# Kernel optimization log

Hardware: AMD Instinct MI355X
Metric: run time of the kernel (lower is better)

The kernel has to match this reference:

```python
import jax, jax.numpy as jnp
import numpy as np

H = 4096          # hidden_size
I = 11008         # intermediate_size
B, S = 4, 2048    # batch, seq_len


def _dequant(wq, scale):
    # per-output-channel symmetric int8 dequant: [out,in] int * [out] scale
    return wq.astype(jnp.float32) * scale[:, None]


def setup_inputs() -> dict:
    key = jax.random.key(0)
    ks = jax.random.split(key, 7)
    x = jax.random.normal(ks[0], (B, S, H), dtype=jnp.float32)
    gate_wq = jax.random.randint(ks[1], (I, H), -127, 128, dtype=jnp.int32)
    up_wq = jax.random.randint(ks[2], (I, H), -127, 128, dtype=jnp.int32)
    down_wq = jax.random.randint(ks[3], (H, I), -127, 128, dtype=jnp.int32)
    # realistic small per-channel scales (~1/127 of a unit-ish weight range)
    gate_scale = jax.random.uniform(ks[4], (I,), dtype=jnp.float32) * 0.01 + 1e-4
    up_scale = jax.random.uniform(ks[5], (I,), dtype=jnp.float32) * 0.01 + 1e-4
    down_scale = jax.random.uniform(ks[6], (H,), dtype=jnp.float32) * 0.01 + 1e-4
    return {
        "x": x,
        "gate_wq": gate_wq, "gate_scale": gate_scale,
        "up_wq": up_wq, "up_scale": up_scale,
        "down_wq": down_wq, "down_scale": down_scale,
    }


def reference(x, gate_wq, gate_scale, up_wq, up_scale, down_wq, down_scale):
    # y = down( gate(x) * up(x) )  -- NOTE: source forward has no activation fn
    gate_w = _dequant(gate_wq, gate_scale)   # [I, H]
    up_w = _dequant(up_wq, up_scale)         # [I, H]
    down_w = _dequant(down_wq, down_scale)   # [H, I]
    g = jnp.einsum('bsh,ih->bsi', x, gate_w)  # [B,S,I]
    u = jnp.einsum('bsh,ih->bsi', x, up_w)    # [B,S,I]
    return jnp.einsum('bsi,hi->bsh', g * u, down_w)  # [B,S,H]
```

## Files before the change

kernel.cpp:

```cpp
#include <hip/hip_runtime.h>


#define H_DIM 4096
#define I_DIM 11008
#define M_DIM 8192

typedef __bf16 bf16;
typedef __bf16 bf16x8 __attribute__((ext_vector_type(8)));
typedef float f32x4 __attribute__((ext_vector_type(4)));

#define GAS __attribute__((address_space(1)))
#define LAS __attribute__((address_space(3)))

__device__ __forceinline__ void async_ld16(const void* g, void* l) {
    __builtin_amdgcn_global_load_lds((const GAS void*)g, (LAS void*)l, 16, 0, 0);
}

__device__ __forceinline__ void barrier_f() {
    asm volatile("" ::: "memory");
    __builtin_amdgcn_s_barrier();
    asm volatile("" ::: "memory");
}

#define WAIT_LGKM0() asm volatile("s_waitcnt lgkmcnt(0)" ::: "memory")
#define WAIT_VM(N)   asm volatile("s_waitcnt vmcnt(" #N ")" ::: "memory")
#define MFMA16 __builtin_amdgcn_mfma_f32_16x16x32_bf16


__global__ __launch_bounds__(256) void cvt_i32_bf16_k(const int* __restrict__ src,
                                                      ushort* __restrict__ dst, int n4) {
    int t = blockIdx.x * 256 + threadIdx.x;
    if (t >= n4) return;
    const int4 v = ((const int4*)src)[t];
    ushort4 o;
    o.x = __builtin_bit_cast(ushort, (bf16)(float)v.x);
    o.y = __builtin_bit_cast(ushort, (bf16)(float)v.y);
    o.z = __builtin_bit_cast(ushort, (bf16)(float)v.z);
    o.w = __builtin_bit_cast(ushort, (bf16)(float)v.w);
    ((ushort4*)dst)[t] = o;
}

__global__ __launch_bounds__(256) void cvt_f32_bf16_k(const float* __restrict__ src,
                                                      ushort* __restrict__ dst, int n4) {
    int t = blockIdx.x * 256 + threadIdx.x;
    if (t >= n4) return;
    const float4 v = ((const float4*)src)[t];
    ushort4 o;
    o.x = __builtin_bit_cast(ushort, (bf16)v.x);
    o.y = __builtin_bit_cast(ushort, (bf16)v.y);
    o.z = __builtin_bit_cast(ushort, (bf16)v.z);
    o.w = __builtin_bit_cast(ushort, (bf16)v.w);
    ((ushort4*)dst)[t] = o;
}


__global__ __launch_bounds__(512, 2) void gemm_gateup(
    const bf16* __restrict__ X, const bf16* __restrict__ WG, const bf16* __restrict__ WU,
    const float* __restrict__ GS, const float* __restrict__ US, ushort* __restrict__ T) {
    __shared__ bf16x8 lds[8192];

    const int tid = threadIdx.x;
    const int lane = tid & 63;
    const int wave = tid >> 6;
    const int wm = wave >> 2, wn = wave & 3;

    const int d = blockIdx.y * gridDim.x + blockIdx.x;
    const int xcd = d & 7, j = d >> 3;
    const int m0 = (xcd * 4 + j / 86) * 256;
    const int i0 = (j % 86) * 128;

    const int srow = tid >> 3;
    const int scol = ((tid & 7) ^ (srow & 7)) * 8;
    const bf16* a_src = X  + (size_t)(m0 + srow) * H_DIM + scol;
    const bf16* g_src = WG + (size_t)(i0 + srow) * H_DIM + scol;
    const bf16* u_src = WU + (size_t)(i0 + srow) * H_DIM + scol;

    auto SA = [&](int kt, int h, int bb) {
        const bf16* s = a_src + (size_t)(h * 128) * H_DIM + kt * 64;
        async_ld16(s, &lds[bb + h * 1024 + tid]);
        async_ld16(s + (size_t)64 * H_DIM, &lds[bb + h * 1024 + 512 + tid]);
    };
    auto SG = [&](int kt, int bb) {
        const bf16* s = g_src + kt * 64;
        async_ld16(s, &lds[bb + 2048 + tid]);
        async_ld16(s + (size_t)64 * H_DIM, &lds[bb + 2048 + 512 + tid]);
    };
    auto SU = [&](int kt, int bb) {
        const bf16* s = u_src + kt * 64;
        async_ld16(s, &lds[bb + 3072 + tid]);
        async_ld16(s + (size_t)64 * H_DIM, &lds[bb + 3072 + 512 + tid]);
    };

    const int l7 = lane & 7, kvh = lane >> 4;
    const int aix = (wm * 128 + (lane & 15)) * 8;
    const int gix = 2048 + (wn * 32 + (lane & 15)) * 8;
    const int uix = 3072 + (wn * 32 + (lane & 15)) * 8;

    f32x4 acc[8][4] = {};

    SA(0, 0, 0); SA(0, 1, 0); SG(0, 0); SU(0, 0);
    SG(1, 4096); SU(1, 4096); SA(1, 0, 4096);
    WAIT_VM(6);
    barrier_f();

    const int NT = H_DIM / 64;
    for (int t = 0; t < NT; ++t) {
        const int cb = (t & 1) << 12;
        const int nb = cb ^ 4096;

        bf16x8 b[4][2], a01[2][2];
#pragma unroll
        for (int j2 = 0; j2 < 2; ++j2)
#pragma unroll
            for (int kk = 0; kk < 2; ++kk) {
                b[j2][kk]     = lds[cb + gix + j2 * 128 + (((kk * 4 + kvh)) ^ l7)];
                b[2 + j2][kk] = lds[cb + uix + j2 * 128 + (((kk * 4 + kvh)) ^ l7)];
            }
#pragma unroll
        for (int mi = 0; mi < 2; ++mi)
#pragma unroll
            for (int kk = 0; kk < 2; ++kk)
                a01[mi][kk] = lds[cb + aix + mi * 128 + (((kk * 4 + kvh)) ^ l7)];
        if (t + 1 < NT) SA(t + 1, 1, nb);
        barrier_f();
        __builtin_amdgcn_s_setprio(1);
#pragma unroll
        for (int mi = 0; mi < 2; ++mi)
#pragma unroll
            for (int j2 = 0; j2 < 4; ++j2)
#pragma unroll
                for (int kk = 0; kk < 2; ++kk)
                    acc[mi][j2] = MFMA16(a01[mi][kk], b[j2][kk], acc[mi][j2], 0, 0, 0);
        __builtin_amdgcn_s_setprio(0);
        barrier_f();

        bf16x8 a23[2][2];
#pragma unroll
        for (int mi = 0; mi < 2; ++mi)
#pragma unroll
            for (int kk = 0; kk < 2; ++kk)
                a23[mi][kk] = lds[cb + aix + (2 + mi) * 128 + (((kk * 4 + kvh)) ^ l7)];
        if (t + 2 < NT) SG(t + 2, cb);
        barrier_f();
        __builtin_amdgcn_s_setprio(1);
#pragma unroll
        for (int mi = 0; mi < 2; ++mi)
#pragma unroll
            for (int j2 = 0; j2 < 4; ++j2)
#pragma unroll
                for (int kk = 0; kk < 2; ++kk)
                    acc[2 + mi][j2] = MFMA16(a23[mi][kk], b[j2][kk], acc[2 + mi][j2], 0, 0, 0);
        __builtin_amdgcn_s_setprio(0);
        barrier_f();

        bf16x8 a47[4][2];
#pragma unroll
        for (int mi = 0; mi < 4; ++mi)
#pragma unroll
            for (int kk = 0; kk < 2; ++kk)
                a47[mi][kk] = lds[cb + aix + (4 + mi) * 128 + (((kk * 4 + kvh)) ^ l7)];
        if (t + 2 < NT) SU(t + 2, cb);
        barrier_f();
        __builtin_amdgcn_s_setprio(1);
#pragma unroll
        for (int mi = 0; mi < 2; ++mi)
#pragma unroll
            for (int j2 = 0; j2 < 4; ++j2)
#pragma unroll
                for (int kk = 0; kk < 2; ++kk)
                    acc[4 + mi][j2] = MFMA16(a47[mi][kk], b[j2][kk], acc[4 + mi][j2], 0, 0, 0);
        __builtin_amdgcn_s_setprio(0);
        WAIT_LGKM0();
        barrier_f();

        if (t + 2 < NT) SA(t + 2, 0, cb);
        barrier_f();
        __builtin_amdgcn_s_setprio(1);
#pragma unroll
        for (int mi = 0; mi < 2; ++mi)
#pragma unroll
            for (int j2 = 0; j2 < 4; ++j2)
#pragma unroll
                for (int kk = 0; kk < 2; ++kk)
                    acc[6 + mi][j2] = MFMA16(a47[2 + mi][kk], b[j2][kk], acc[6 + mi][j2], 0, 0, 0);
        __builtin_amdgcn_s_setprio(0);
        if (t + 2 < NT) { WAIT_VM(6); } else { WAIT_VM(0); }
        barrier_f();
    }

#pragma unroll
    for (int j2 = 0; j2 < 2; ++j2) {
        const int col = i0 + wn * 32 + j2 * 16 + (lane & 15);
        const float gsv = GS[col], usv = US[col];
#pragma unroll
        for (int mi = 0; mi < 8; ++mi) {
            const int row0 = m0 + wm * 128 + mi * 16 + (lane >> 4) * 4;
#pragma unroll
            for (int r = 0; r < 4; ++r) {
                float g = acc[mi][j2][r] * gsv;
                float u = acc[mi][2 + j2][r] * usv;
                T[(size_t)(row0 + r) * I_DIM + col] = __builtin_bit_cast(ushort, (bf16)(g * u));
            }
        }
    }
}


__global__ __launch_bounds__(512, 2) void gemm_down(
    const bf16* __restrict__ T, const bf16* __restrict__ WD,
    const float* __restrict__ DS, float* __restrict__ Y) {
    __shared__ bf16x8 lds[8192];

    const int tid = threadIdx.x;
    const int lane = tid & 63;
    const int wave = tid >> 6;
    const int wm = wave >> 2, wn = wave & 3;

    const int d = blockIdx.y * gridDim.x + blockIdx.x;
    const int xcd = d & 7, j = d >> 3;
    const int m0 = (xcd * 4 + j / 16) * 256;
    const int n0 = (j % 16) * 256;

    const int srow = tid >> 3;
    const int scol = ((tid & 7) ^ (srow & 7)) * 8;
    const bf16* a_src = T  + (size_t)(m0 + srow) * I_DIM + scol;
    const bf16* b_src = WD + (size_t)(n0 + srow) * I_DIM + scol;

    auto SA = [&](int kt, int h, int bb) {
        const bf16* s = a_src + (size_t)(h * 128) * I_DIM + kt * 64;
        async_ld16(s, &lds[bb + h * 1024 + tid]);
        async_ld16(s + (size_t)64 * I_DIM, &lds[bb + h * 1024 + 512 + tid]);
    };
    auto SB = [&](int kt, int h, int bb) {
        const bf16* s = b_src + (size_t)(h * 128) * I_DIM + kt * 64;
        async_ld16(s, &lds[bb + 2048 + h * 1024 + tid]);
        async_ld16(s + (size_t)64 * I_DIM, &lds[bb + 2048 + h * 1024 + 512 + tid]);
    };

    const int l7 = lane & 7, kvh = lane >> 4;
    const int aix = (wm * 128 + (lane & 15)) * 8;
    const int bix = 2048 + ((wn >> 1) * 128 + (wn & 1) * 64 + (lane & 15)) * 8;

    f32x4 acc[8][4] = {};

    SA(0, 0, 0); SA(0, 1, 0); SB(0, 0, 0); SB(0, 1, 0);
    SB(1, 0, 4096); SB(1, 1, 4096); SA(1, 0, 4096);
    WAIT_VM(6);
    barrier_f();

    const int NT = I_DIM / 64;
    for (int t = 0; t < NT; ++t) {
        const int cb = (t & 1) << 12;
        const int nb = cb ^ 4096;

        bf16x8 b[4][2], a01[2][2];
#pragma unroll
        for (int j2 = 0; j2 < 4; ++j2)
#pragma unroll
            for (int kk = 0; kk < 2; ++kk)
                b[j2][kk] = lds[cb + bix + j2 * 128 + (((kk * 4 + kvh)) ^ l7)];
#pragma unroll
        for (int mi = 0; mi < 2; ++mi)
#pragma unroll
            for (int kk = 0; kk < 2; ++kk)
                a01[mi][kk] = lds[cb + aix + mi * 128 + (((kk * 4 + kvh)) ^ l7)];
        if (t + 1 < NT) SA(t + 1, 1, nb);
        barrier_f();
        __builtin_amdgcn_s_setprio(1);
#pragma unroll
        for (int mi = 0; mi < 2; ++mi)
#pragma unroll
            for (int j2 = 0; j2 < 4; ++j2)
#pragma unroll
                for (int kk = 0; kk < 2; ++kk)
                    acc[mi][j2] = MFMA16(a01[mi][kk], b[j2][kk], acc[mi][j2], 0, 0, 0);
        __builtin_amdgcn_s_setprio(0);
        barrier_f();

        bf16x8 a23[2][2];
#pragma unroll
        for (int mi = 0; mi < 2; ++mi)
#pragma unroll
            for (int kk = 0; kk < 2; ++kk)
                a23[mi][kk] = lds[cb + aix + (2 + mi) * 128 + (((kk * 4 + kvh)) ^ l7)];
        if (t + 2 < NT) SB(t + 2, 0, cb);
        barrier_f();
        __builtin_amdgcn_s_setprio(1);
#pragma unroll
        for (int mi = 0; mi < 2; ++mi)
#pragma unroll
            for (int j2 = 0; j2 < 4; ++j2)
#pragma unroll
                for (int kk = 0; kk < 2; ++kk)
                    acc[2 + mi][j2] = MFMA16(a23[mi][kk], b[j2][kk], acc[2 + mi][j2], 0, 0, 0);
        __builtin_amdgcn_s_setprio(0);
        barrier_f();

        bf16x8 a47[4][2];
#pragma unroll
        for (int mi = 0; mi < 4; ++mi)
#pragma unroll
            for (int kk = 0; kk < 2; ++kk)
                a47[mi][kk] = lds[cb + aix + (4 + mi) * 128 + (((kk * 4 + kvh)) ^ l7)];
        if (t + 2 < NT) SB(t + 2, 1, cb);
        barrier_f();
        __builtin_amdgcn_s_setprio(1);
#pragma unroll
        for (int mi = 0; mi < 2; ++mi)
#pragma unroll
            for (int j2 = 0; j2 < 4; ++j2)
#pragma unroll
                for (int kk = 0; kk < 2; ++kk)
                    acc[4 + mi][j2] = MFMA16(a47[mi][kk], b[j2][kk], acc[4 + mi][j2], 0, 0, 0);
        __builtin_amdgcn_s_setprio(0);
        WAIT_LGKM0();
        barrier_f();

        if (t + 2 < NT) SA(t + 2, 0, cb);
        barrier_f();
        __builtin_amdgcn_s_setprio(1);
#pragma unroll
        for (int mi = 0; mi < 2; ++mi)
#pragma unroll
            for (int j2 = 0; j2 < 4; ++j2)
#pragma unroll
                for (int kk = 0; kk < 2; ++kk)
                    acc[6 + mi][j2] = MFMA16(a47[2 + mi][kk], b[j2][kk], acc[6 + mi][j2], 0, 0, 0);
        __builtin_amdgcn_s_setprio(0);
        if (t + 2 < NT) { WAIT_VM(6); } else { WAIT_VM(0); }
        barrier_f();
    }

#pragma unroll
    for (int j2 = 0; j2 < 4; ++j2) {
        const int col = n0 + wn * 64 + j2 * 16 + (lane & 15);
        const float dsv = DS[col];
#pragma unroll
        for (int mi = 0; mi < 8; ++mi) {
            const int row0 = m0 + wm * 128 + mi * 16 + (lane >> 4) * 4;
#pragma unroll
            for (int r = 0; r < 4; ++r)
                Y[(size_t)(row0 + r) * H_DIM + col] = acc[mi][j2][r] * dsv;
        }
    }
}


extern "C" void kernel_launch(void* const* d_in, const int* in_sizes, int n_in,
                              void* d_out, int out_size, void* d_ws, size_t ws_size,
                              hipStream_t stream) {
    const float* x   = (const float*)d_in[0];
    const int*   gwq = (const int*)d_in[1];
    const float* gs  = (const float*)d_in[2];
    const int*   uwq = (const int*)d_in[3];
    const float* us  = (const float*)d_in[4];
    const int*   dwq = (const int*)d_in[5];
    const float* ds  = (const float*)d_in[6];
    float* y = (float*)d_out;

    char* ws = (char*)d_ws;
    bf16*   ws_x  = (bf16*)(ws);
    bf16*   ws_gw = (bf16*)(ws + 67108864ull);
    bf16*   ws_uw = (bf16*)(ws + 157286400ull);
    bf16*   ws_dw = (bf16*)(ws + 247463936ull);
    ushort* ws_t  = (ushort*)(ws + 337641472ull);

    const int nx4 = M_DIM * H_DIM / 4;
    const int nw4 = I_DIM * H_DIM / 4;

    cvt_f32_bf16_k<<<nx4 / 256, 256, 0, stream>>>(x, (ushort*)ws_x, nx4);
    cvt_i32_bf16_k<<<nw4 / 256, 256, 0, stream>>>(gwq, (ushort*)ws_gw, nw4);
    cvt_i32_bf16_k<<<nw4 / 256, 256, 0, stream>>>(uwq, (ushort*)ws_uw, nw4);
    cvt_i32_bf16_k<<<nw4 / 256, 256, 0, stream>>>(dwq, (ushort*)ws_dw, nw4);

    gemm_gateup<<<dim3(M_DIM / 256, I_DIM / 128), 512, 0, stream>>>(ws_x, ws_gw, ws_uw, gs, us, ws_t);
    gemm_down<<<dim3(M_DIM / 256, H_DIM / 256), 512, 0, stream>>>((const bf16*)ws_t, ws_dw, ds, y);
}
```

Measured before the change: 2.299 ms.

## Restructure GEMM main loops from four to three phases, issuing prefetches in pairs

Both GEMM kernels now run each K-tile in three compute phases instead of four. All A-fragment LDS reads are hoisted into the second phase, and the global-to-LDS prefetches are grouped into two paired issues (gate+up or B halves, then both A halves). The separate next-buffer A-half prefetch is removed, and the vmcnt waits are adjusted to match. The aim is fewer barriers per iteration and longer uninterrupted MFMA runs, at the cost of more live registers and a prefetch distance whose stalls may be less well hidden.

```diff
diff --git a/kernel.cpp b/kernel.cpp
--- a/kernel.cpp
+++ b/kernel.cpp
@@ -99,14 +99,13 @@
     f32x4 acc[8][4] = {};
 
     SA(0, 0, 0); SA(0, 1, 0); SG(0, 0); SU(0, 0);
-    SG(1, 4096); SU(1, 4096); SA(1, 0, 4096);
-    WAIT_VM(6);
+    SG(1, 4096); SU(1, 4096); SA(1, 0, 4096); SA(1, 1, 4096);
+    WAIT_VM(8);
     barrier_f();
 
     const int NT = H_DIM / 64;
     for (int t = 0; t < NT; ++t) {
         const int cb = (t & 1) << 12;
-        const int nb = cb ^ 4096;
 
         bf16x8 b[4][2], a01[2][2];
 #pragma unroll
@@ -121,7 +120,6 @@
 #pragma unroll
             for (int kk = 0; kk < 2; ++kk)
                 a01[mi][kk] = lds[cb + aix + mi * 128 + (((kk * 4 + kvh)) ^ l7)];
-        if (t + 1 < NT) SA(t + 1, 1, nb);
         barrier_f();
         __builtin_amdgcn_s_setprio(1);
 #pragma unroll
@@ -134,13 +132,19 @@
         __builtin_amdgcn_s_setprio(0);
         barrier_f();
 
-        bf16x8 a23[2][2];
+        bf16x8 a23[2][2], a47[4][2];
 #pragma unroll
         for (int mi = 0; mi < 2; ++mi)
 #pragma unroll
             for (int kk = 0; kk < 2; ++kk)
                 a23[mi][kk] = lds[cb + aix + (2 + mi) * 128 + (((kk * 4 + kvh)) ^ l7)];
-        if (t + 2 < NT) SG(t + 2, cb);
+#pragma unroll
+        for (int mi = 0; mi < 4; ++mi)
+#pragma unroll
+            for (int kk = 0; kk < 2; ++kk)
+                a47[mi][kk] = lds[cb + aix + (4 + mi) * 128 + (((kk * 4 + kvh)) ^ l7)];
+        if (t + 2 < NT) { SG(t + 2, cb); SU(t + 2, cb); }
+        WAIT_LGKM0();
         barrier_f();
         __builtin_amdgcn_s_setprio(1);
 #pragma unroll
@@ -153,38 +157,17 @@
         __builtin_amdgcn_s_setprio(0);
         barrier_f();
 
-        bf16x8 a47[4][2];
+        if (t + 2 < NT) { SA(t + 2, 0, cb); SA(t + 2, 1, cb); }
+        __builtin_amdgcn_s_setprio(1);
 #pragma unroll
         for (int mi = 0; mi < 4; ++mi)
 #pragma unroll
-            for (int kk = 0; kk < 2; ++kk)
-                a47[mi][kk] = lds[cb + aix + (4 + mi) * 128 + (((kk * 4 + kvh)) ^ l7)];
-        if (t + 2 < NT) SU(t + 2, cb);
-        barrier_f();
-        __builtin_amdgcn_s_setprio(1);
-#pragma unroll
-        for (int mi = 0; mi < 2; ++mi)
-#pragma unroll
             for (int j2 = 0; j2 < 4; ++j2)
 #pragma unroll
                 for (int kk = 0; kk < 2; ++kk)
                     acc[4 + mi][j2] = MFMA16(a47[mi][kk], b[j2][kk], acc[4 + mi][j2], 0, 0, 0);
         __builtin_amdgcn_s_setprio(0);
-        WAIT_LGKM0();
-        barrier_f();
-
-        if (t + 2 < NT) SA(t + 2, 0, cb);
-        barrier_f();
-        __builtin_amdgcn_s_setprio(1);
-#pragma unroll
-        for (int mi = 0; mi < 2; ++mi)
-#pragma unroll
-            for (int j2 = 0; j2 < 4; ++j2)
-#pragma unroll
-                for (int kk = 0; kk < 2; ++kk)
-                    acc[6 + mi][j2] = MFMA16(a47[2 + mi][kk], b[j2][kk], acc[6 + mi][j2], 0, 0, 0);
-        __builtin_amdgcn_s_setprio(0);
-        if (t + 2 < NT) { WAIT_VM(6); } else { WAIT_VM(0); }
+        if (t + 2 < NT) { WAIT_VM(8); } else { WAIT_VM(0); }
         barrier_f();
     }
 
@@ -244,14 +227,13 @@
     f32x4 acc[8][4] = {};
 
     SA(0, 0, 0); SA(0, 1, 0); SB(0, 0, 0); SB(0, 1, 0);
-    SB(1, 0, 4096); SB(1, 1, 4096); SA(1, 0, 4096);
-    WAIT_VM(6);
+    SB(1, 0, 4096); SB(1, 1, 4096); SA(1, 0, 4096); SA(1, 1, 4096);
+    WAIT_VM(8);
     barrier_f();
 
     const int NT = I_DIM / 64;
     for (int t = 0; t < NT; ++t) {
         const int cb = (t & 1) << 12;
-        const int nb = cb ^ 4096;
 
         bf16x8 b[4][2], a01[2][2];
 #pragma unroll
@@ -264,7 +246,6 @@
 #pragma unroll
             for (int kk = 0; kk < 2; ++kk)
                 a01[mi][kk] = lds[cb + aix + mi * 128 + (((kk * 4 + kvh)) ^ l7)];
-        if (t + 1 < NT) SA(t + 1, 1, nb);
         barrier_f();
         __builtin_amdgcn_s_setprio(1);
 #pragma unroll
@@ -277,13 +258,19 @@
         __builtin_amdgcn_s_setprio(0);
         barrier_f();
 
-        bf16x8 a23[2][2];
+        bf16x8 a23[2][2], a47[4][2];
 #pragma unroll
         for (int mi = 0; mi < 2; ++mi)
 #pragma unroll
             for (int kk = 0; kk < 2; ++kk)
                 a23[mi][kk] = lds[cb + aix + (2 + mi) * 128 + (((kk * 4 + kvh)) ^ l7)];
-        if (t + 2 < NT) SB(t + 2, 0, cb);
+#pragma unroll
+        for (int mi = 0; mi < 4; ++mi)
+#pragma unroll
+            for (int kk = 0; kk < 2; ++kk)
+                a47[mi][kk] = lds[cb + aix + (4 + mi) * 128 + (((kk * 4 + kvh)) ^ l7)];
+        if (t + 2 < NT) { SB(t + 2, 0, cb); SB(t + 2, 1, cb); }
+        WAIT_LGKM0();
         barrier_f();
         __builtin_amdgcn_s_setprio(1);
 #pragma unroll
@@ -296,38 +283,17 @@
         __builtin_amdgcn_s_setprio(0);
         barrier_f();
 
-        bf16x8 a47[4][2];
+        if (t + 2 < NT) { SA(t + 2, 0, cb); SA(t + 2, 1, cb); }
+        __builtin_amdgcn_s_setprio(1);
 #pragma unroll
         for (int mi = 0; mi < 4; ++mi)
 #pragma unroll
-            for (int kk = 0; kk < 2; ++kk)
-                a47[mi][kk] = lds[cb + aix + (4 + mi) * 128 + (((kk * 4 + kvh)) ^ l7)];
-        if (t + 2 < NT) SB(t + 2, 1, cb);
-        barrier_f();
-        __builtin_amdgcn_s_setprio(1);
-#pragma unroll
-        for (int mi = 0; mi < 2; ++mi)
-#pragma unroll
             for (int j2 = 0; j2 < 4; ++j2)
 #pragma unroll
                 for (int kk = 0; kk < 2; ++kk)
                     acc[4 + mi][j2] = MFMA16(a47[mi][kk], b[j2][kk], acc[4 + mi][j2], 0, 0, 0);
         __builtin_amdgcn_s_setprio(0);
-        WAIT_LGKM0();
-        barrier_f();
-
-        if (t + 2 < NT) SA(t + 2, 0, cb);
-        barrier_f();
-        __builtin_amdgcn_s_setprio(1);
-#pragma unroll
-        for (int mi = 0; mi < 2; ++mi)
-#pragma unroll
-            for (int j2 = 0; j2 < 4; ++j2)
-#pragma unroll
-                for (int kk = 0; kk < 2; ++kk)
-                    acc[6 + mi][j2] = MFMA16(a47[2 + mi][kk], b[j2][kk], acc[6 + mi][j2], 0, 0, 0);
-        __builtin_amdgcn_s_setprio(0);
-        if (t + 2 < NT) { WAIT_VM(6); } else { WAIT_VM(0); }
+        if (t + 2 < NT) { WAIT_VM(8); } else { WAIT_VM(0); }
         barrier_f();
     }
 
```

Result: slower. 2.403 ms (+4.5%).
